# Kernel optimization log

Measured on AMD Instinct MI355X. Metric: run time of the kernel, lower is better.

## Reference

```python
import jax, jax.numpy as jnp
import numpy as np
from jax import lax

T, K, F = 262144, 20, 16


def setup_inputs() -> dict:
    key = jax.random.key(0)
    k1, k2, k3, k4 = jax.random.split(key, 4)
    return {
        "observations": jax.random.normal(k1, (T, F), dtype=jnp.float32),
        "beta_logits": jax.random.normal(k2, (K,), dtype=jnp.float32),
        "pi_logits": jax.random.normal(k3, (K, K), dtype=jnp.float32),
        "means": jax.random.normal(k4, (K, F), dtype=jnp.float32),
        "log_vars": jnp.zeros((K, F), dtype=jnp.float32),
    }


def _stick_breaking(logits):
    b = jax.nn.sigmoid(logits)
    cp = jnp.cumprod(1.0 - b)
    return b * jnp.concatenate([jnp.ones((1,), logits.dtype), cp[:-1]])


def _emission_logp(obs, means, log_vars):
    # Diagonal-covariance MultivariateNormal log_prob, vectorized over T and K
    # without materializing a [T,K,F] intermediate.
    var = jnp.exp(log_vars) + 1e-6                       # [K,F]
    inv = 1.0 / var
    const = jnp.sum(means * means * inv + jnp.log(2.0 * jnp.pi * var), axis=1)  # [K]
    quad = (obs * obs) @ inv.T - 2.0 * (obs @ (means * inv).T)                  # [T,K]
    return -0.5 * (quad + const[None, :])


def reference(observations, beta_logits, pi_logits, means, log_vars):
    w = _stick_breaking(beta_logits)                      # [K]
    P = jax.nn.softmax(pi_logits, axis=1)                 # [K,K]
    em = _emission_logp(observations, means, log_vars)    # [T,K]

    # Forward recursion (normalized alpha, as in the original)
    a0 = w * jnp.exp(em[0])
    a0 = a0 / (a0.sum() + 1e-10)

    def fstep(a, e):
        x = (a @ P) * jnp.exp(e)
        x = x / (x.sum() + 1e-10)
        return x, x

    _, a_rest = lax.scan(fstep, a0, em[1:])
    alpha = jnp.concatenate([a0[None], a_rest], axis=0)   # [T,K]

    # Backward recursion (normalized beta)
    bT = jnp.ones((K,), observations.dtype)

    def bstep(bn, e):
        x = P @ (bn * jnp.exp(e))
        x = x / (x.sum() + 1e-10)
        return x, x

    _, b_rest = lax.scan(bstep, bT, em[1:], reverse=True)
    beta = jnp.concatenate([b_rest, bT[None]], axis=0)    # [T,K]

    log_likelihood = jnp.log(alpha[-1].sum() + 1e-10)
    return alpha, beta, log_likelihood
```

## Files before the change

### kernel.cpp

```cpp
#include <hip/hip_runtime.h>
#include <hip/hip_fp16.h>


namespace {
constexpr int Tn = 262144;
constexpr int Kn = 20;
constexpr int Fn = 16;
constexpr float EPSF = 1e-10f;
constexpr float TINY = 1e-35f;

constexpr int Ln3 = 16;
constexpr int Wn3 = 16;
constexpr int NC3 = Tn / Ln3;
constexpr int NBF4 = NC3 / 32;
constexpr int NBSC = NC3 / 8;
constexpr int SPC = Ln3 * Kn;

constexpr size_t OFF_P    = 0;
constexpr size_t OFF_W    = 400;
constexpr size_t OFF_CK   = 420;
constexpr size_t OFF_MVIV = 440;
constexpr size_t OFF_E    = 1152;
constexpr size_t OFF_MF   = OFF_E + (size_t)Tn*20 + 64;
constexpr size_t OFF_MB   = OFF_MF + (size_t)Tn;
constexpr size_t OFF_MATF = OFF_MB + (size_t)Tn;
constexpr size_t OFF_MATB = OFF_MATF + 4*(size_t)NC3;
constexpr size_t OFF_SF   = OFF_MATB + 4*(size_t)NC3;
constexpr size_t OFF_SB   = OFF_SF + NC3;
constexpr size_t OFF_END  = OFF_SB + NC3;
}

#if __has_builtin(__builtin_amdgcn_rcpf)
#define FRCP(x) __builtin_amdgcn_rcpf(x)
#else
#define FRCP(x) (1.0f/(x))
#endif

template<int CTRL>
__device__ __forceinline__ float dpp_add(float v) {
  int s = __builtin_amdgcn_update_dpp(0, __float_as_int(v), CTRL, 0xF, 0xF, true);
  return v + __int_as_float(s);
}
template<int CTRL>
__device__ __forceinline__ float dppmov(float v) {
  return __int_as_float(__builtin_amdgcn_update_dpp(0, __float_as_int(v), CTRL, 0xF, 0xF, true));
}

__device__ __forceinline__ float reduce8(float v) {
  v = dpp_add<0xB1>(v);
  v = dpp_add<0x4E>(v);
  v = dpp_add<0x141>(v);
  return v;
}

__global__ __launch_bounds__(64) void prep_kernel(
    const float* beta_logits, const float* pi_logits,
    const float* means, const float* log_vars, float* ws)
{
  int k = threadIdx.x;
  if (k < Kn) {
    float row[Kn];
    float mx = -1e30f;
#pragma unroll
    for (int j = 0; j < Kn; ++j) { row[j] = pi_logits[k*Kn + j]; mx = fmaxf(mx, row[j]); }
    float s = 0.f;
#pragma unroll
    for (int j = 0; j < Kn; ++j) { row[j] = expf(row[j] - mx); s += row[j]; }
    float invs = 1.0f / s;
#pragma unroll
    for (int j = 0; j < Kn; ++j) ws[OFF_P + k*Kn + j] = row[j] * invs;
    float ck = 0.f;
#pragma unroll
    for (int f = 0; f < Fn; ++f) {
      float lv  = log_vars[k*Fn + f];
      float var = expf(lv) + 1e-6f;
      float iv  = 1.0f / var;
      float mu  = means[k*Fn + f];
      ((float2*)(ws + OFF_MVIV))[k*Fn + f] = make_float2(mu * iv, iv);
      ck += mu*mu*iv + logf(6.2831853071795864f * var);
    }
    ws[OFF_CK + k] = ck;
  } else if (k == Kn) {
    float cp = 1.f;
#pragma unroll
    for (int i = 0; i < Kn; ++i) {
      float b = 1.0f / (1.0f + expf(-beta_logits[i]));
      ws[OFF_W + i] = b * cp;
      cp *= (1.0f - b);
    }
  }
}

__global__ __launch_bounds__(320) void emis_kernel(const float* __restrict__ obs, float* ws)
{
  __shared__ __align__(16) float so[64][20];
  __shared__ __align__(16) float scm[16][24];
  __shared__ __align__(16) float scv[16][24];
  __shared__ __align__(16) float sck[20];
  const int tid = threadIdx.x;
  const int t0 = blockIdx.x * 64;

  if (tid < 256) {
    float4 v = ((const float4*)(obs + (size_t)t0 * Fn))[tid];
    int r = tid >> 2, j = tid & 3;
    *(float4*)&so[r][j*4] = v;
  } else {
    int i = tid - 256;
#pragma unroll
    for (int q = 0; q < 5; ++q) {
      int idx = i * 5 + q;
      float2 c2 = ((const float2*)(ws + OFF_MVIV))[idx];
      int k = idx >> 4, f = idx & 15;
      scm[f][k] = c2.x;
      scv[f][k] = c2.y;
    }
    if (i < Kn) sck[i] = ws[OFF_CK + i];
  }
  __syncthreads();

  const int tl = tid / 5;
  const int k0 = (tid - tl*5) * 4;

  float o[16];
  *(float4*)&o[0]  = *(const float4*)&so[tl][0];
  *(float4*)&o[4]  = *(const float4*)&so[tl][4];
  *(float4*)&o[8]  = *(const float4*)&so[tl][8];
  *(float4*)&o[12] = *(const float4*)&so[tl][12];

  float s1x=0.f,s1y=0.f,s1z=0.f,s1w=0.f;
  float s2x=0.f,s2y=0.f,s2z=0.f,s2w=0.f;
#pragma unroll
  for (int f = 0; f < Fn; ++f) {
    float4 cm = *(const float4*)&scm[f][k0];
    float4 cv = *(const float4*)&scv[f][k0];
    float ov = o[f];
    s1x = fmaf(cv.x * ov, ov, s1x); s2x = fmaf(cm.x, ov, s2x);
    s1y = fmaf(cv.y * ov, ov, s1y); s2y = fmaf(cm.y, ov, s2y);
    s1z = fmaf(cv.z * ov, ov, s1z); s2z = fmaf(cm.z, ov, s2z);
    s1w = fmaf(cv.w * ov, ov, s1w); s2w = fmaf(cm.w, ov, s2w);
  }
  float4 ckv = *(const float4*)&sck[k0];
  float4 rr;
  rr.x = __expf(fmaf(-0.5f, s1x + ckv.x, s2x));
  rr.y = __expf(fmaf(-0.5f, s1y + ckv.y, s2y));
  rr.z = __expf(fmaf(-0.5f, s1z + ckv.z, s2z));
  rr.w = __expf(fmaf(-0.5f, s1w + ckv.w, s2w));
  *(float4*)(ws + OFF_E + (size_t)(t0 + tl)*20 + k0) = rr;
}

__global__ __launch_bounds__(256, 4) void scan5_kernel(float* ws, float* out)
{
  const int tid = threadIdx.x;
  const int g   = tid >> 3;
  const int j   = tid & 7;
  const int q   = j & 3;
  const int s1i = 8 + j;
  const int s2i = 16 + q;
  const bool isF = ((int)blockIdx.x < NBF4);
  const int c = (isF ? (int)blockIdx.x : (int)blockIdx.x - NBF4) * 32 + g;
  const float* E = ws + OFF_E;

  float PA0[8], PB0[8], PA1[8], PB1[8], PA2[8], PB2[8];
  float PC0[4], PC1[4], PC2[4];
  {
    const int M[8] = {0,1,2,3,7,6,5,4};
#pragma unroll
    for (int i = 0; i < 8; ++i) {
      int ka = j ^ M[i];
      int kb = 8 + ka;
      if (isF) {
        PA0[i] = ws[OFF_P + ka*Kn + j];
        PB0[i] = ws[OFF_P + kb*Kn + j];
        PA1[i] = ws[OFF_P + ka*Kn + s1i];
        PB1[i] = ws[OFF_P + kb*Kn + s1i];
        PA2[i] = ws[OFF_P + ka*Kn + s2i];
        PB2[i] = ws[OFF_P + kb*Kn + s2i];
      } else {
        PA0[i] = ws[OFF_P + j*Kn + ka];
        PB0[i] = ws[OFF_P + j*Kn + kb];
        PA1[i] = ws[OFF_P + s1i*Kn + ka];
        PB1[i] = ws[OFF_P + s1i*Kn + kb];
        PA2[i] = ws[OFF_P + s2i*Kn + ka];
        PB2[i] = ws[OFF_P + s2i*Kn + kb];
      }
    }
#pragma unroll
    for (int i = 0; i < 4; ++i) {
      int kc = 16 + (q ^ i);
      if (isF) {
        PC0[i] = ws[OFF_P + kc*Kn + j];
        PC1[i] = ws[OFF_P + kc*Kn + s1i];
        PC2[i] = ws[OFF_P + kc*Kn + s2i];
      } else {
        PC0[i] = ws[OFF_P + j*Kn + kc];
        PC1[i] = ws[OFF_P + s1i*Kn + kc];
        PC2[i] = ws[OFF_P + s2i*Kn + kc];
      }
    }
  }

  float Ma = 1.f, Mc = 0.f, Md = 1.f;
  float* mArr = ws + (isF ? OFF_MF : OFF_MB);
  unsigned* uS = (unsigned*)(out + (isF ? (size_t)0 : (size_t)Tn * Kn) + (size_t)c * SPC);

  auto mobius = [&](float m) {
    float na = m * Ma;
    float nc = fmaf(EPSF, Mc, na);
    float nd = EPSF * Md;
    float mx = fmaxf(nc, nd);
    float lam = (mx > 0.f) ? FRCP(mx) : 1.0f;
    Ma = na*lam; Mc = nc*lam; Md = nd*lam;
  };

  auto packh2 = [](float a, float b) -> unsigned {
    __half2 h2 = __floats2half2_rn(a, b);
    return *(unsigned*)&h2;
  };

  auto xmv = [&](float w0, float w1, float w2, float& r0, float& r1, float& r2) {
    float x10 = dppmov<0xB1>(w0),  x11 = dppmov<0xB1>(w1),  x12 = dppmov<0xB1>(w2);
    float x20 = dppmov<0x4E>(w0),  x21 = dppmov<0x4E>(w1),  x22 = dppmov<0x4E>(w2);
    float x30 = dppmov<0x1B>(w0),  x31 = dppmov<0x1B>(w1),  x32 = dppmov<0x1B>(w2);
    float m0  = dppmov<0x141>(w0), m1  = dppmov<0x141>(w1);
    float m01 = dppmov<0xB1>(m0),  m11 = dppmov<0xB1>(m1);
    float m02 = dppmov<0x4E>(m0),  m12 = dppmov<0x4E>(m1);
    float m03 = dppmov<0x1B>(m0),  m13 = dppmov<0x1B>(m1);
#define ACC3(PA, PB, PC, OUT)                                             \
    {                                                                     \
      float a  = w0 * PA[0],  b = x10 * PA[1];                            \
      a = fmaf(x20, PA[2], a); b = fmaf(x30, PA[3], b);                   \
      a = fmaf(m0,  PA[4], a); b = fmaf(m01, PA[5], b);                   \
      a = fmaf(m02, PA[6], a); b = fmaf(m03, PA[7], b);                   \
      a = fmaf(w1,  PB[0], a); b = fmaf(x11, PB[1], b);                   \
      a = fmaf(x21, PB[2], a); b = fmaf(x31, PB[3], b);                   \
      a = fmaf(m1,  PB[4], a); b = fmaf(m11, PB[5], b);                   \
      a = fmaf(m12, PB[6], a); b = fmaf(m13, PB[7], b);                   \
      a = fmaf(w2,  PC[0], a); b = fmaf(x12, PC[1], b);                   \
      a = fmaf(x22, PC[2], a); b = fmaf(x32, PC[3], b);                   \
      OUT = a + b;                                                        \
    }
    ACC3(PA0, PB0, PC0, r0)
    ACC3(PA1, PB1, PC1, r1)
    ACC3(PA2, PB2, PC2, r2)
#undef ACC3
  };

  if (isF) {
    const int bodyStart = c * Ln3;
    const int tend = bodyStart + Ln3 - 1;
    const int t0 = (c == 0) ? 0 : (bodyStart - Wn3);
    float e0a = E[t0*20 + j], e1a = E[t0*20 + s1i], e2a = E[t0*20 + s2i];
    float v0, v1, v2;
    if (c == 0) {
      v0 = ws[OFF_W + j]   * e0a;
      v1 = ws[OFF_W + s1i] * e1a;
      v2 = ws[OFF_W + s2i] * e2a;
    } else {
      v0 = 0.05f * e0a; v1 = 0.05f * e1a; v2 = 0.05f * e2a;
    }
    float sv = reduce8(fmaf(0.5f, v2, v0 + v1));
    float m = sv;
    float iV = (sv > TINY) ? FRCP(sv) : 1.0f;
    if (sv <= TINY) { v0 = 0.05f; v1 = 0.05f; v2 = 0.05f; }
    if (c == 0) {
      mArr[0] = m;
      mobius(m);
      uS[j] = packh2(v0 * iV, v1 * iV);
      uS[8 + q] = packh2(v2 * iV, 0.f);
    }
    float A = m * iV;
    float rho = (m > TINY) ? FRCP(m) : 1.0f;
    float e0b = E[(t0+1)*20 + j], e1b = E[(t0+1)*20 + s1i], e2b = E[(t0+1)*20 + s2i];
    float e0c = E[(t0+2)*20 + j], e1c = E[(t0+2)*20 + s1i], e2c = E[(t0+2)*20 + s2i];

#define FWD_STEP(REC)                                                     \
    {                                                                     \
      float acc0, acc1, acc2;                                             \
      xmv(v0, v1, v2, acc0, acc1, acc2);                                  \
      float er0 = e0a * rho, er1 = e1a * rho, er2 = e2a * rho;            \
      e0a = e0b; e0b = e0c; e0c = E[(t+3)*20 + j];                        \
      e1a = e1b; e1b = e1c; e1c = E[(t+3)*20 + s1i];                      \
      e2a = e2b; e2b = e2c; e2c = E[(t+3)*20 + s2i];                      \
      v0 = acc0 * er0; v1 = acc1 * er1; v2 = acc2 * er2;                  \
      float sv2 = reduce8(fmaf(0.5f, v2, v0 + v1));                      \
      float mn = sv2 * A;                                                 \
      float iVn = (sv2 > TINY) ? FRCP(sv2) : 1.0f;                        \
      if (sv2 <= TINY) { v0 = 0.05f; v1 = 0.05f; v2 = 0.05f; }            \
      if (REC) {                                                          \
        mArr[t] = mn;                                                     \
        mobius(mn);                                                       \
        int lt = t - bodyStart;                                           \
        uS[lt*12 + j] = packh2(v0 * iVn, v1 * iVn);                       \
        uS[lt*12 + 8 + q] = packh2(v2 * iVn, 0.f);                        \
      }                                                                   \
      A = mn * iVn;                                                       \
      rho = (mn > TINY) ? FRCP(mn) : 1.0f;                                \
    }

    for (int t = t0 + 1; t < bodyStart; ++t) FWD_STEP(false)
    const int bstart2 = (c == 0) ? 1 : bodyStart;
    for (int t = bstart2; t <= tend; ++t) FWD_STEP(true)
#undef FWD_STEP
    ((float4*)(ws + OFF_MATF))[c] = make_float4(Ma, Mc, Md, 0.f);
  } else {
    const int bodyStart = c * Ln3;
    const int top = bodyStart + Ln3 - 1;
    int r0 = top + Wn3; if (r0 > Tn - 1) r0 = Tn - 1;
    float v0 = 0.05f, v1 = 0.05f, v2 = 0.05f;
    float sv = reduce8(fmaf(0.5f, v2, v0 + v1));
    float iV = (sv > TINY) ? FRCP(sv) : 1.0f;
    float A = iV;
    float rho = 1.0f;
    float e0a = E[r0*20 + j], e1a = E[r0*20 + s1i], e2a = E[r0*20 + s2i];
    float e0b = E[(r0-1)*20 + j], e1b = E[(r0-1)*20 + s1i], e2b = E[(r0-1)*20 + s2i];
    float e0c = E[(r0-2)*20 + j], e1c = E[(r0-2)*20 + s1i], e2c = E[(r0-2)*20 + s2i];

#define BWD_STEP(REC)                                                     \
    {                                                                     \
      float w0 = v0 * e0a, w1 = v1 * e1a, w2 = v2 * e2a;                  \
      float acc0, acc1, acc2;                                             \
      xmv(w0, w1, w2, acc0, acc1, acc2);                                  \
      v0 = acc0 * rho; v1 = acc1 * rho; v2 = acc2 * rho;                  \
      e0a = e0b; e0b = e0c; e0c = E[(r-2)*20 + j];                        \
      e1a = e1b; e1b = e1c; e1c = E[(r-2)*20 + s1i];                      \
      e2a = e2b; e2b = e2c; e2c = E[(r-2)*20 + s2i];                      \
      float sv2 = reduce8(fmaf(0.5f, v2, v0 + v1));                      \
      float mn = sv2 * A;                                                 \
      float iVn = (sv2 > TINY) ? FRCP(sv2) : 1.0f;                        \
      if (sv2 <= TINY) { v0 = 0.05f; v1 = 0.05f; v2 = 0.05f; }            \
      if (REC) {                                                          \
        mArr[r+1] = mn;                                                   \
        mobius(mn);                                                       \
        int lr = r - bodyStart;                                           \
        uS[lr*12 + j] = packh2(v0 * iVn, v1 * iVn);                       \
        uS[lr*12 + 8 + q] = packh2(v2 * iVn, 0.f);                        \
      }                                                                   \
      A = mn * iVn;                                                       \
      rho = (mn > TINY) ? FRCP(mn) : 1.0f;                                \
    }

    for (int r = r0 - 1; r > top; --r) BWD_STEP(false)
    int rb = (r0 - 1 < top) ? (r0 - 1) : top;
    for (int r = rb; r >= bodyStart; --r) BWD_STEP(true)
#undef BWD_STEP
    ((float4*)(ws + OFF_MATB))[NC3 - 1 - c] = make_float4(Ma, Mc, Md, 0.f);
  }
}

__global__ __launch_bounds__(1024) void combine4_kernel(float* ws, float* out)
{
  __shared__ float wag[16][3];
  __shared__ float wpre[16][3];
  const bool isF = (blockIdx.x == 0);
  const float4* M4 = (const float4*)(ws + (isF ? OFF_MATF : OFF_MATB));
  float* sArr = ws + (isF ? OFF_SF : OFF_SB);
  const float s0 = isF ? 1.0f : 20.0f;
  constexpr int PG = NC3 / 1024;
  const int tid  = threadIdx.x;
  const int lane = tid & 63;
  const int wid  = tid >> 6;

  float4 mm[PG];
#pragma unroll
  for (int i = 0; i < PG; ++i) mm[i] = M4[tid*PG + i];

  float a = 1.f, cc = 0.f, d = 1.f;
#pragma unroll
  for (int i = 0; i < PG; ++i) {
    float na = mm[i].x * a;
    float nc = fmaf(mm[i].y, a, mm[i].z * cc);
    float nd = mm[i].z * d;
    float mx = fmaxf(na, fmaxf(nc, nd));
    float lam = (mx > 0.f) ? FRCP(mx) : 1.0f;
    a = na*lam; cc = nc*lam; d = nd*lam;
  }

  float ia = a, ic = cc, id = d;
  for (int off = 1; off < 64; off <<= 1) {
    float pa = __shfl_up(ia, off, 64);
    float pc = __shfl_up(ic, off, 64);
    float pd = __shfl_up(id, off, 64);
    if (lane >= off) {
      float na = ia * pa;
      float nc = fmaf(ic, pa, id * pc);
      float nd = id * pd;
      float mx = fmaxf(na, fmaxf(nc, nd));
      float lam = (mx > 0.f) ? FRCP(mx) : 1.0f;
      ia = na*lam; ic = nc*lam; id = nd*lam;
    }
  }
  if (lane == 63) { wag[wid][0] = ia; wag[wid][1] = ic; wag[wid][2] = id; }
  __syncthreads();

  if (tid == 0) {
    float ea = 1.f, ec = 0.f, ed = 1.f;
#pragma unroll
    for (int w = 0; w < 16; ++w) {
      wpre[w][0] = ea; wpre[w][1] = ec; wpre[w][2] = ed;
      float na = wag[w][0] * ea;
      float nc = fmaf(wag[w][1], ea, wag[w][2] * ec);
      float nd = wag[w][2] * ed;
      float mx = fmaxf(na, fmaxf(nc, nd));
      float lam = (mx > 0.f) ? FRCP(mx) : 1.0f;
      ea = na*lam; ec = nc*lam; ed = nd*lam;
    }
    if (isF) {
      float den = fmaf(ec, s0, ed);
      float sfin = (den > 0.f) ? (ea * s0)/den : 0.f;
      out[(size_t)2 * Tn * Kn] = logf(sfin + EPSF);
    }
  }
  __syncthreads();

  float ea = __shfl_up(ia, 1, 64);
  float ec = __shfl_up(ic, 1, 64);
  float ed = __shfl_up(id, 1, 64);
  if (lane == 0) { ea = 1.f; ec = 0.f; ed = 1.f; }
  float pa = wpre[wid][0], pc = wpre[wid][1], pd = wpre[wid][2];
  float xa = ea * pa;
  float xc = fmaf(ec, pa, ed * pc);
  float xd = ed * pd;

  float num = xa * s0, den = fmaf(xc, s0, xd);
  float s = (den > 0.f) ? num/den : 0.f;
#pragma unroll
  for (int i = 0; i < PG; ++i) {
    sArr[tid*PG + i] = s;
    float nn = mm[i].x * s, dd = fmaf(mm[i].y, s, mm[i].z);
    s = (dd > 0.f) ? nn/dd : 0.f;
  }
}

__global__ __launch_bounds__(128) void scale4_kernel(float* ws, float* out)
{
  const int tid = threadIdx.x;
  const int g   = tid >> 4;
  const int ll  = tid & 15;
  const bool isF = ((int)blockIdx.x < NBSC);
  const int c = (isF ? (int)blockIdx.x : (int)blockIdx.x - NBSC) * 8 + g;
  float* base = out + (isF ? (size_t)0 : (size_t)Tn * Kn) + (size_t)c * SPC;
  const unsigned* uS = (const unsigned*)base;

  float mySig = 1.0f;
  if (isF) {
    const float* mA = ws + OFF_MF;
    float s = ws[OFF_SF + c];
    const int t0 = c * Ln3;
#pragma unroll
    for (int i = 0; i < Ln3; ++i) {
      float z = s * mA[t0 + i];
      float sn = z * FRCP(z + EPSF);
      if (i == ll) mySig = sn;
      s = sn;
    }
  } else {
    const float* mA = ws + OFF_MB;
    float s = ws[OFF_SB + (NC3 - 1 - c)];
    const int top = c * Ln3 + Ln3 - 1;
#pragma unroll
    for (int i = 0; i < Ln3; ++i) {
      int r = top - i;
      float sn;
      if (r == Tn - 1) sn = s;
      else {
        float z = s * mA[r + 1];
        sn = z * FRCP(z + EPSF);
      }
      if (i == Ln3 - 1 - ll) mySig = sn;
      s = sn;
    }
  }

  uint4 ua = ((const uint4*)(uS + ll*12))[0];
  uint4 ub = ((const uint4*)(uS + ll*12))[1];
  uint4 uc = ((const uint4*)(uS + ll*12))[2];
  __syncthreads();

  const bool onesRow = (!isF && c == NC3 - 1 && ll == Ln3 - 1);
  float sg = mySig;
  unsigned slots[12] = {ua.x,ua.y,ua.z,ua.w, ub.x,ub.y,ub.z,ub.w, uc.x,uc.y,uc.z,uc.w};
  float o[20];
#pragma unroll
  for (int jj = 0; jj < 8; ++jj) {
    __half2 h2 = *(__half2*)&slots[jj];
    float2 f2 = __half22float2(h2);
    o[jj]     = f2.x * sg;
    o[8 + jj] = f2.y * sg;
  }
#pragma unroll
  for (int qq = 0; qq < 4; ++qq) {
    __half2 h2 = *(__half2*)&slots[8 + qq];
    float2 f2 = __half22float2(h2);
    o[16 + qq] = f2.x * sg;
  }
  if (onesRow) {
#pragma unroll
    for (int k = 0; k < 20; ++k) o[k] = 1.0f;
  }
  float* dst = base + ll * 20;
  *(float4*)&dst[0]  = *(float4*)&o[0];
  *(float4*)&dst[4]  = *(float4*)&o[4];
  *(float4*)&dst[8]  = *(float4*)&o[8];
  *(float4*)&dst[12] = *(float4*)&o[12];
  *(float4*)&dst[16] = *(float4*)&o[16];
}

extern "C" void kernel_launch(void* const* d_in, const int* in_sizes, int n_in,
                              void* d_out, int out_size, void* d_ws, size_t ws_size,
                              hipStream_t stream) {
  const float* obs         = (const float*)d_in[0];
  const float* beta_logits = (const float*)d_in[1];
  const float* pi_logits   = (const float*)d_in[2];
  const float* means       = (const float*)d_in[3];
  const float* log_vars    = (const float*)d_in[4];
  float* out = (float*)d_out;
  float* ws  = (float*)d_ws;

  hipLaunchKernelGGL(prep_kernel, dim3(1), dim3(64), 0, stream,
                     beta_logits, pi_logits, means, log_vars, ws);
  hipLaunchKernelGGL(emis_kernel, dim3(Tn/64), dim3(320), 0, stream, obs, ws);
  hipLaunchKernelGGL(scan5_kernel, dim3(2*NBF4), dim3(256), 0, stream, ws, out);
  hipLaunchKernelGGL(combine4_kernel, dim3(2), dim3(1024), 0, stream, ws, out);
  hipLaunchKernelGGL(scale4_kernel, dim3(2*NBSC), dim3(128), 0, stream, ws, out);
}
```

Before: 102.0 us.

## Halve scan warm-up window and deepen emission prefetch pipeline

The forward and backward chunked scans now run an 8-step warm-up window before each 16-step chunk body instead of 16 steps. This cuts the redundant recomputation per chunk by roughly a third. Emission values are also prefetched four steps ahead instead of three, to hide more global-load latency. The shorter window relies on the HMM forgetting its initial state within 8 steps, so it may reduce accuracy of the chunk-boundary approximation.

```diff
diff --git a/kernel.cpp b/kernel.cpp
--- a/kernel.cpp
+++ b/kernel.cpp
@@ -10,7 +10,7 @@
 constexpr float TINY = 1e-35f;
 
 constexpr int Ln3 = 16;
-constexpr int Wn3 = 16;
+constexpr int Wn3 = 8;
 constexpr int NC3 = Tn / Ln3;
 constexpr int NBF4 = NC3 / 32;
 constexpr int NBSC = NC3 / 8;
@@ -148,7 +148,7 @@
   *(float4*)(ws + OFF_E + (size_t)(t0 + tl)*20 + k0) = rr;
 }
 
-__global__ __launch_bounds__(256, 4) void scan5_kernel(float* ws, float* out)
+__global__ __launch_bounds__(256, 4) void scan6_kernel(float* ws, float* out)
 {
   const int tid = threadIdx.x;
   const int g   = tid >> 3;
@@ -211,12 +211,10 @@
     float lam = (mx > 0.f) ? FRCP(mx) : 1.0f;
     Ma = na*lam; Mc = nc*lam; Md = nd*lam;
   };
-
   auto packh2 = [](float a, float b) -> unsigned {
     __half2 h2 = __floats2half2_rn(a, b);
     return *(unsigned*)&h2;
   };
-
   auto xmv = [&](float w0, float w1, float w2, float& r0, float& r1, float& r2) {
     float x10 = dppmov<0xB1>(w0),  x11 = dppmov<0xB1>(w1),  x12 = dppmov<0xB1>(w2);
     float x20 = dppmov<0x4E>(w0),  x21 = dppmov<0x4E>(w1),  x22 = dppmov<0x4E>(w2);
@@ -249,14 +247,16 @@
     const int bodyStart = c * Ln3;
     const int tend = bodyStart + Ln3 - 1;
     const int t0 = (c == 0) ? 0 : (bodyStart - Wn3);
-    float e0a = E[t0*20 + j], e1a = E[t0*20 + s1i], e2a = E[t0*20 + s2i];
     float v0, v1, v2;
-    if (c == 0) {
-      v0 = ws[OFF_W + j]   * e0a;
-      v1 = ws[OFF_W + s1i] * e1a;
-      v2 = ws[OFF_W + s2i] * e2a;
-    } else {
-      v0 = 0.05f * e0a; v1 = 0.05f * e1a; v2 = 0.05f * e2a;
+    {
+      float e0i = E[t0*20 + j], e1i = E[t0*20 + s1i], e2i = E[t0*20 + s2i];
+      if (c == 0) {
+        v0 = ws[OFF_W + j]   * e0i;
+        v1 = ws[OFF_W + s1i] * e1i;
+        v2 = ws[OFF_W + s2i] * e2i;
+      } else {
+        v0 = 0.05f * e0i; v1 = 0.05f * e1i; v2 = 0.05f * e2i;
+      }
     }
     float sv = reduce8(fmaf(0.5f, v2, v0 + v1));
     float m = sv;
@@ -270,17 +270,19 @@
     }
     float A = m * iV;
     float rho = (m > TINY) ? FRCP(m) : 1.0f;
-    float e0b = E[(t0+1)*20 + j], e1b = E[(t0+1)*20 + s1i], e2b = E[(t0+1)*20 + s2i];
-    float e0c = E[(t0+2)*20 + j], e1c = E[(t0+2)*20 + s1i], e2c = E[(t0+2)*20 + s2i];
+    float e0a = E[(t0+1)*20 + j], e1a = E[(t0+1)*20 + s1i], e2a = E[(t0+1)*20 + s2i];
+    float e0b = E[(t0+2)*20 + j], e1b = E[(t0+2)*20 + s1i], e2b = E[(t0+2)*20 + s2i];
+    float e0c = E[(t0+3)*20 + j], e1c = E[(t0+3)*20 + s1i], e2c = E[(t0+3)*20 + s2i];
+    float e0d = E[(t0+4)*20 + j], e1d = E[(t0+4)*20 + s1i], e2d = E[(t0+4)*20 + s2i];
 
 #define FWD_STEP(REC)                                                     \
     {                                                                     \
       float acc0, acc1, acc2;                                             \
       xmv(v0, v1, v2, acc0, acc1, acc2);                                  \
       float er0 = e0a * rho, er1 = e1a * rho, er2 = e2a * rho;            \
-      e0a = e0b; e0b = e0c; e0c = E[(t+3)*20 + j];                        \
-      e1a = e1b; e1b = e1c; e1c = E[(t+3)*20 + s1i];                      \
-      e2a = e2b; e2b = e2c; e2c = E[(t+3)*20 + s2i];                      \
+      e0a = e0b; e0b = e0c; e0c = e0d; e0d = E[(t+4)*20 + j];             \
+      e1a = e1b; e1b = e1c; e1c = e1d; e1d = E[(t+4)*20 + s1i];           \
+      e2a = e2b; e2b = e2c; e2c = e2d; e2d = E[(t+4)*20 + s2i];           \
       v0 = acc0 * er0; v1 = acc1 * er1; v2 = acc2 * er2;                  \
       float sv2 = reduce8(fmaf(0.5f, v2, v0 + v1));                      \
       float mn = sv2 * A;                                                 \
@@ -311,9 +313,10 @@
     float iV = (sv > TINY) ? FRCP(sv) : 1.0f;
     float A = iV;
     float rho = 1.0f;
-    float e0a = E[r0*20 + j], e1a = E[r0*20 + s1i], e2a = E[r0*20 + s2i];
+    float e0a = E[r0*20 + j],     e1a = E[r0*20 + s1i],     e2a = E[r0*20 + s2i];
     float e0b = E[(r0-1)*20 + j], e1b = E[(r0-1)*20 + s1i], e2b = E[(r0-1)*20 + s2i];
     float e0c = E[(r0-2)*20 + j], e1c = E[(r0-2)*20 + s1i], e2c = E[(r0-2)*20 + s2i];
+    float e0d = E[(r0-3)*20 + j], e1d = E[(r0-3)*20 + s1i], e2d = E[(r0-3)*20 + s2i];
 
 #define BWD_STEP(REC)                                                     \
     {                                                                     \
@@ -321,9 +324,9 @@
       float acc0, acc1, acc2;                                             \
       xmv(w0, w1, w2, acc0, acc1, acc2);                                  \
       v0 = acc0 * rho; v1 = acc1 * rho; v2 = acc2 * rho;                  \
-      e0a = e0b; e0b = e0c; e0c = E[(r-2)*20 + j];                        \
-      e1a = e1b; e1b = e1c; e1c = E[(r-2)*20 + s1i];                      \
-      e2a = e2b; e2b = e2c; e2c = E[(r-2)*20 + s2i];                      \
+      e0a = e0b; e0b = e0c; e0c = e0d; e0d = E[(r-3)*20 + j];             \
+      e1a = e1b; e1b = e1c; e1c = e1d; e1d = E[(r-3)*20 + s1i];           \
+      e2a = e2b; e2b = e2c; e2c = e2d; e2d = E[(r-3)*20 + s2i];           \
       float sv2 = reduce8(fmaf(0.5f, v2, v0 + v1));                      \
       float mn = sv2 * A;                                                 \
       float iVn = (sv2 > TINY) ? FRCP(sv2) : 1.0f;                        \
@@ -519,7 +522,7 @@
   hipLaunchKernelGGL(prep_kernel, dim3(1), dim3(64), 0, stream,
                      beta_logits, pi_logits, means, log_vars, ws);
   hipLaunchKernelGGL(emis_kernel, dim3(Tn/64), dim3(320), 0, stream, obs, ws);
-  hipLaunchKernelGGL(scan5_kernel, dim3(2*NBF4), dim3(256), 0, stream, ws, out);
+  hipLaunchKernelGGL(scan6_kernel, dim3(2*NBF4), dim3(256), 0, stream, ws, out);
   hipLaunchKernelGGL(combine4_kernel, dim3(2), dim3(1024), 0, stream, ws, out);
   hipLaunchKernelGGL(scale4_kernel, dim3(2*NBSC), dim3(128), 0, stream, ws, out);
 }
```

After: 99.01 us. -2.9%, faster.

## Fuse prep into consumers, halve warmup window, interleave two chunks per thread group

Applied to the files above, without the earlier changes.

Removes the separate prep kernel. Emission parameters are now computed inside emis_kernel, and the transition matrix and stick-breaking weights are computed into shared memory inside the scan kernel. The scan warmup window drops from 16 to 8 steps. Each 8-lane group now processes two adjacent chunks in one interleaved loop, giving independent instruction streams that hide DPP and reduce latency. In exchange, the work per block is duplicated, register pressure rises (the occupancy hint is dropped), and the shorter warmup may reduce accuracy at chunk boundaries.

```diff
diff --git a/kernel.cpp b/kernel.cpp
--- a/kernel.cpp
+++ b/kernel.cpp
@@ -10,18 +10,14 @@
 constexpr float TINY = 1e-35f;
 
 constexpr int Ln3 = 16;
-constexpr int Wn3 = 16;
+constexpr int Wn3 = 8;
 constexpr int NC3 = Tn / Ln3;
-constexpr int NBF4 = NC3 / 32;
+constexpr int NBF8 = NC3 / 2 / 32;
 constexpr int NBSC = NC3 / 8;
 constexpr int SPC = Ln3 * Kn;
 
-constexpr size_t OFF_P    = 0;
-constexpr size_t OFF_W    = 400;
-constexpr size_t OFF_CK   = 420;
-constexpr size_t OFF_MVIV = 440;
-constexpr size_t OFF_E    = 1152;
-constexpr size_t OFF_MF   = OFF_E + (size_t)Tn*20 + 64;
+constexpr size_t OFF_E    = 256;
+constexpr size_t OFF_MF   = OFF_E + (size_t)Tn*20 + 256;
 constexpr size_t OFF_MB   = OFF_MF + (size_t)Tn;
 constexpr size_t OFF_MATF = OFF_MB + (size_t)Tn;
 constexpr size_t OFF_MATB = OFF_MATF + 4*(size_t)NC3;
@@ -53,45 +49,14 @@
   return v;
 }
 
-__global__ __launch_bounds__(64) void prep_kernel(
-    const float* beta_logits, const float* pi_logits,
-    const float* means, const float* log_vars, float* ws)
-{
-  int k = threadIdx.x;
-  if (k < Kn) {
-    float row[Kn];
-    float mx = -1e30f;
-#pragma unroll
-    for (int j = 0; j < Kn; ++j) { row[j] = pi_logits[k*Kn + j]; mx = fmaxf(mx, row[j]); }
-    float s = 0.f;
-#pragma unroll
-    for (int j = 0; j < Kn; ++j) { row[j] = expf(row[j] - mx); s += row[j]; }
-    float invs = 1.0f / s;
-#pragma unroll
-    for (int j = 0; j < Kn; ++j) ws[OFF_P + k*Kn + j] = row[j] * invs;
-    float ck = 0.f;
-#pragma unroll
-    for (int f = 0; f < Fn; ++f) {
-      float lv  = log_vars[k*Fn + f];
-      float var = expf(lv) + 1e-6f;
-      float iv  = 1.0f / var;
-      float mu  = means[k*Fn + f];
-      ((float2*)(ws + OFF_MVIV))[k*Fn + f] = make_float2(mu * iv, iv);
-      ck += mu*mu*iv + logf(6.2831853071795864f * var);
-    }
-    ws[OFF_CK + k] = ck;
-  } else if (k == Kn) {
-    float cp = 1.f;
-#pragma unroll
-    for (int i = 0; i < Kn; ++i) {
-      float b = 1.0f / (1.0f + expf(-beta_logits[i]));
-      ws[OFF_W + i] = b * cp;
-      cp *= (1.0f - b);
-    }
-  }
-}
-
-__global__ __launch_bounds__(320) void emis_kernel(const float* __restrict__ obs, float* ws)
+__device__ __forceinline__ unsigned packh2(float a, float b) {
+  __half2 h2 = __floats2half2_rn(a, b);
+  return *(unsigned*)&h2;
+}
+
+__global__ __launch_bounds__(320) void emis_kernel(
+    const float* __restrict__ obs, const float* __restrict__ means,
+    const float* __restrict__ log_vars, float* ws)
 {
   __shared__ __align__(16) float so[64][20];
   __shared__ __align__(16) float scm[16][24];
@@ -106,15 +71,20 @@
     *(float4*)&so[r][j*4] = v;
   } else {
     int i = tid - 256;
-#pragma unroll
-    for (int q = 0; q < 5; ++q) {
-      int idx = i * 5 + q;
-      float2 c2 = ((const float2*)(ws + OFF_MVIV))[idx];
-      int k = idx >> 4, f = idx & 15;
-      scm[f][k] = c2.x;
-      scv[f][k] = c2.y;
-    }
-    if (i < Kn) sck[i] = ws[OFF_CK + i];
+    if (i < Kn) {
+      float ck = 0.f;
+#pragma unroll
+      for (int f = 0; f < Fn; ++f) {
+        float lv  = log_vars[i*Fn + f];
+        float var = expf(lv) + 1e-6f;
+        float iv  = 1.0f / var;
+        float mu  = means[i*Fn + f];
+        scm[f][i] = mu * iv;
+        scv[f][i] = iv;
+        ck += mu*mu*iv + logf(6.2831853071795864f * var);
+      }
+      sck[i] = ck;
+    }
   }
   __syncthreads();
 
@@ -148,16 +118,42 @@
   *(float4*)(ws + OFF_E + (size_t)(t0 + tl)*20 + k0) = rr;
 }
 
-__global__ __launch_bounds__(256, 4) void scan5_kernel(float* ws, float* out)
+__global__ __launch_bounds__(256) void scan8_kernel(
+    const float* __restrict__ beta_logits, const float* __restrict__ pi_logits,
+    float* ws, float* out)
 {
+  __shared__ __align__(16) float Psh[Kn*Kn];
+  __shared__ float wsh[Kn];
   const int tid = threadIdx.x;
+  if (tid < Kn) {
+    float row[Kn]; float mx = -1e30f;
+#pragma unroll
+    for (int jj = 0; jj < Kn; ++jj) { row[jj] = pi_logits[tid*Kn + jj]; mx = fmaxf(mx, row[jj]); }
+    float s = 0.f;
+#pragma unroll
+    for (int jj = 0; jj < Kn; ++jj) { row[jj] = expf(row[jj] - mx); s += row[jj]; }
+    float invs = 1.0f / s;
+#pragma unroll
+    for (int jj = 0; jj < Kn; ++jj) Psh[tid*Kn + jj] = row[jj] * invs;
+  } else if (tid == Kn) {
+    float cp = 1.f;
+#pragma unroll
+    for (int i = 0; i < Kn; ++i) {
+      float b = 1.0f / (1.0f + expf(-beta_logits[i]));
+      wsh[i] = b * cp;
+      cp *= (1.0f - b);
+    }
+  }
+  __syncthreads();
+
   const int g   = tid >> 3;
   const int j   = tid & 7;
   const int q   = j & 3;
   const int s1i = 8 + j;
   const int s2i = 16 + q;
-  const bool isF = ((int)blockIdx.x < NBF4);
-  const int c = (isF ? (int)blockIdx.x : (int)blockIdx.x - NBF4) * 32 + g;
+  const bool isF = ((int)blockIdx.x < NBF8);
+  const int pairI = (isF ? (int)blockIdx.x : (int)blockIdx.x - NBF8) * 32 + g;
+  const int cA = pairI * 2, cB = cA + 1;
   const float* E = ws + OFF_E;
 
   float PA0[8], PB0[8], PA1[8], PB1[8], PA2[8], PB2[8];
@@ -169,41 +165,33 @@
       int ka = j ^ M[i];
       int kb = 8 + ka;
       if (isF) {
-        PA0[i] = ws[OFF_P + ka*Kn + j];
-        PB0[i] = ws[OFF_P + kb*Kn + j];
-        PA1[i] = ws[OFF_P + ka*Kn + s1i];
-        PB1[i] = ws[OFF_P + kb*Kn + s1i];
-        PA2[i] = ws[OFF_P + ka*Kn + s2i];
-        PB2[i] = ws[OFF_P + kb*Kn + s2i];
+        PA0[i] = Psh[ka*Kn + j];   PB0[i] = Psh[kb*Kn + j];
+        PA1[i] = Psh[ka*Kn + s1i]; PB1[i] = Psh[kb*Kn + s1i];
+        PA2[i] = Psh[ka*Kn + s2i]; PB2[i] = Psh[kb*Kn + s2i];
       } else {
-        PA0[i] = ws[OFF_P + j*Kn + ka];
-        PB0[i] = ws[OFF_P + j*Kn + kb];
-        PA1[i] = ws[OFF_P + s1i*Kn + ka];
-        PB1[i] = ws[OFF_P + s1i*Kn + kb];
-        PA2[i] = ws[OFF_P + s2i*Kn + ka];
-        PB2[i] = ws[OFF_P + s2i*Kn + kb];
+        PA0[i] = Psh[j*Kn + ka];   PB0[i] = Psh[j*Kn + kb];
+        PA1[i] = Psh[s1i*Kn + ka]; PB1[i] = Psh[s1i*Kn + kb];
+        PA2[i] = Psh[s2i*Kn + ka]; PB2[i] = Psh[s2i*Kn + kb];
       }
     }
 #pragma unroll
     for (int i = 0; i < 4; ++i) {
       int kc = 16 + (q ^ i);
       if (isF) {
-        PC0[i] = ws[OFF_P + kc*Kn + j];
-        PC1[i] = ws[OFF_P + kc*Kn + s1i];
-        PC2[i] = ws[OFF_P + kc*Kn + s2i];
+        PC0[i] = Psh[kc*Kn + j]; PC1[i] = Psh[kc*Kn + s1i]; PC2[i] = Psh[kc*Kn + s2i];
       } else {
-        PC0[i] = ws[OFF_P + j*Kn + kc];
-        PC1[i] = ws[OFF_P + s1i*Kn + kc];
-        PC2[i] = ws[OFF_P + s2i*Kn + kc];
+        PC0[i] = Psh[j*Kn + kc]; PC1[i] = Psh[s1i*Kn + kc]; PC2[i] = Psh[s2i*Kn + kc];
       }
     }
   }
-
-  float Ma = 1.f, Mc = 0.f, Md = 1.f;
+  const float w0c = wsh[j], w1c = wsh[s1i], w2c = wsh[s2i];
+
+  float MaA=1.f, McA=0.f, MdA=1.f, MaB=1.f, McB=0.f, MdB=1.f;
   float* mArr = ws + (isF ? OFF_MF : OFF_MB);
-  unsigned* uS = (unsigned*)(out + (isF ? (size_t)0 : (size_t)Tn * Kn) + (size_t)c * SPC);
-
-  auto mobius = [&](float m) {
+  unsigned* uSA = (unsigned*)(out + (isF ? (size_t)0 : (size_t)Tn * Kn) + (size_t)cA * SPC);
+  unsigned* uSB = uSA + SPC;
+
+  auto mobius = [&](float m, float& Ma, float& Mc, float& Md) {
     float na = m * Ma;
     float nc = fmaf(EPSF, Mc, na);
     float nd = EPSF * Md;
@@ -211,12 +199,6 @@
     float lam = (mx > 0.f) ? FRCP(mx) : 1.0f;
     Ma = na*lam; Mc = nc*lam; Md = nd*lam;
   };
-
-  auto packh2 = [](float a, float b) -> unsigned {
-    __half2 h2 = __floats2half2_rn(a, b);
-    return *(unsigned*)&h2;
-  };
-
   auto xmv = [&](float w0, float w1, float w2, float& r0, float& r1, float& r2) {
     float x10 = dppmov<0xB1>(w0),  x11 = dppmov<0xB1>(w1),  x12 = dppmov<0xB1>(w2);
     float x20 = dppmov<0x4E>(w0),  x21 = dppmov<0x4E>(w1),  x22 = dppmov<0x4E>(w2);
@@ -246,104 +228,147 @@
   };
 
   if (isF) {
-    const int bodyStart = c * Ln3;
-    const int tend = bodyStart + Ln3 - 1;
-    const int t0 = (c == 0) ? 0 : (bodyStart - Wn3);
-    float e0a = E[t0*20 + j], e1a = E[t0*20 + s1i], e2a = E[t0*20 + s2i];
-    float v0, v1, v2;
-    if (c == 0) {
-      v0 = ws[OFF_W + j]   * e0a;
-      v1 = ws[OFF_W + s1i] * e1a;
-      v2 = ws[OFF_W + s2i] * e2a;
-    } else {
-      v0 = 0.05f * e0a; v1 = 0.05f * e1a; v2 = 0.05f * e2a;
-    }
-    float sv = reduce8(fmaf(0.5f, v2, v0 + v1));
-    float m = sv;
-    float iV = (sv > TINY) ? FRCP(sv) : 1.0f;
-    if (sv <= TINY) { v0 = 0.05f; v1 = 0.05f; v2 = 0.05f; }
-    if (c == 0) {
-      mArr[0] = m;
-      mobius(m);
-      uS[j] = packh2(v0 * iV, v1 * iV);
-      uS[8 + q] = packh2(v2 * iV, 0.f);
-    }
-    float A = m * iV;
-    float rho = (m > TINY) ? FRCP(m) : 1.0f;
-    float e0b = E[(t0+1)*20 + j], e1b = E[(t0+1)*20 + s1i], e2b = E[(t0+1)*20 + s2i];
-    float e0c = E[(t0+2)*20 + j], e1c = E[(t0+2)*20 + s1i], e2c = E[(t0+2)*20 + s2i];
-
-#define FWD_STEP(REC)                                                     \
-    {                                                                     \
-      float acc0, acc1, acc2;                                             \
-      xmv(v0, v1, v2, acc0, acc1, acc2);                                  \
-      float er0 = e0a * rho, er1 = e1a * rho, er2 = e2a * rho;            \
-      e0a = e0b; e0b = e0c; e0c = E[(t+3)*20 + j];                        \
-      e1a = e1b; e1b = e1c; e1c = E[(t+3)*20 + s1i];                      \
-      e2a = e2b; e2b = e2c; e2c = E[(t+3)*20 + s2i];                      \
-      v0 = acc0 * er0; v1 = acc1 * er1; v2 = acc2 * er2;                  \
-      float sv2 = reduce8(fmaf(0.5f, v2, v0 + v1));                      \
-      float mn = sv2 * A;                                                 \
-      float iVn = (sv2 > TINY) ? FRCP(sv2) : 1.0f;                        \
-      if (sv2 <= TINY) { v0 = 0.05f; v1 = 0.05f; v2 = 0.05f; }            \
-      if (REC) {                                                          \
-        mArr[t] = mn;                                                     \
-        mobius(mn);                                                       \
-        int lt = t - bodyStart;                                           \
-        uS[lt*12 + j] = packh2(v0 * iVn, v1 * iVn);                       \
-        uS[lt*12 + 8 + q] = packh2(v2 * iVn, 0.f);                        \
-      }                                                                   \
-      A = mn * iVn;                                                       \
-      rho = (mn > TINY) ? FRCP(mn) : 1.0f;                                \
-    }
-
-    for (int t = t0 + 1; t < bodyStart; ++t) FWD_STEP(false)
-    const int bstart2 = (c == 0) ? 1 : bodyStart;
-    for (int t = bstart2; t <= tend; ++t) FWD_STEP(true)
-#undef FWD_STEP
-    ((float4*)(ws + OFF_MATF))[c] = make_float4(Ma, Mc, Md, 0.f);
+    const int bSA = cA * Ln3;
+    const bool c0 = (cA == 0);
+    float vA0, vA1, vA2, vB0, vB1, vB2;
+    {
+      const float* p0 = E + (ptrdiff_t)(bSA - 8) * 20;
+      vA0 = 0.05f * p0[j]; vA1 = 0.05f * p0[s1i]; vA2 = 0.05f * p0[s2i];
+      const float* p1 = E + (ptrdiff_t)(bSA + 8) * 20;
+      vB0 = 0.05f * p1[j]; vB1 = 0.05f * p1[s1i]; vB2 = 0.05f * p1[s2i];
+    }
+    float svA = reduce8(fmaf(0.5f, vA2, vA0 + vA1));
+    float iVA = (svA > TINY) ? FRCP(svA) : 1.0f;
+    if (svA <= TINY) { vA0 = vA1 = vA2 = 0.05f; }
+    float AA = svA * iVA;
+    float rhoA = (svA > TINY) ? FRCP(svA) : 1.0f;
+    float svB = reduce8(fmaf(0.5f, vB2, vB0 + vB1));
+    float iVB = (svB > TINY) ? FRCP(svB) : 1.0f;
+    if (svB <= TINY) { vB0 = vB1 = vB2 = 0.05f; }
+    float AB = svB * iVB;
+    float rhoB = (svB > TINY) ? FRCP(svB) : 1.0f;
+
+    const float* pA = E + (ptrdiff_t)(bSA - 7) * 20;
+    float eA0a = pA[j], eA1a = pA[s1i], eA2a = pA[s2i]; pA += 20;
+    float eA0b = pA[j], eA1b = pA[s1i], eA2b = pA[s2i]; pA += 20;
+    float eA0c = pA[j], eA1c = pA[s1i], eA2c = pA[s2i]; pA += 20;
+    const float* pB = E + (ptrdiff_t)(bSA + 9) * 20;
+    float eB0a = pB[j], eB1a = pB[s1i], eB2a = pB[s2i]; pB += 20;
+    float eB0b = pB[j], eB1b = pB[s1i], eB2b = pB[s2i]; pB += 20;
+    float eB0c = pB[j], eB1c = pB[s1i], eB2c = pB[s2i]; pB += 20;
+
+    for (int i = 0; i < 23; ++i) {
+      const int t = bSA - 7 + i;
+      float accA0, accA1, accA2, accB0, accB1, accB2;
+      xmv(vA0, vA1, vA2, accA0, accA1, accA2);
+      xmv(vB0, vB1, vB2, accB0, accB1, accB2);
+      float ea0 = eA0a, ea1 = eA1a, ea2 = eA2a;
+      float eb0 = eB0a, eb1 = eB1a, eb2 = eB2a;
+      eA0a = eA0b; eA0b = eA0c; eA0c = pA[j];
+      eA1a = eA1b; eA1b = eA1c; eA1c = pA[s1i];
+      eA2a = eA2b; eA2b = eA2c; eA2c = pA[s2i]; pA += 20;
+      eB0a = eB0b; eB0b = eB0c; eB0c = pB[j];
+      eB1a = eB1b; eB1b = eB1c; eB1c = pB[s1i];
+      eB2a = eB2b; eB2b = eB2c; eB2c = pB[s2i]; pB += 20;
+      const bool init0 = c0 && (t == 0);
+      vA0 = init0 ? (w0c * ea0) : (accA0 * (ea0 * rhoA));
+      vA1 = init0 ? (w1c * ea1) : (accA1 * (ea1 * rhoA));
+      vA2 = init0 ? (w2c * ea2) : (accA2 * (ea2 * rhoA));
+      vB0 = accB0 * (eb0 * rhoB);
+      vB1 = accB1 * (eb1 * rhoB);
+      vB2 = accB2 * (eb2 * rhoB);
+      float sA = reduce8(fmaf(0.5f, vA2, vA0 + vA1));
+      float sB = reduce8(fmaf(0.5f, vB2, vB0 + vB1));
+      float mnA = sA * (init0 ? 1.0f : AA);
+      float mnB = sB * AB;
+      float iVnA = (sA > TINY) ? FRCP(sA) : 1.0f;
+      float iVnB = (sB > TINY) ? FRCP(sB) : 1.0f;
+      if (sA <= TINY) { vA0 = vA1 = vA2 = 0.05f; }
+      if (sB <= TINY) { vB0 = vB1 = vB2 = 0.05f; }
+      if (i >= 7) {
+        const int lt = i - 7;
+        mArr[t] = mnA;
+        mArr[t + 16] = mnB;
+        mobius(mnA, MaA, McA, MdA);
+        mobius(mnB, MaB, McB, MdB);
+        uSA[lt*12 + j] = packh2(vA0 * iVnA, vA1 * iVnA);
+        uSA[lt*12 + 8 + q] = packh2(vA2 * iVnA, 0.f);
+        uSB[lt*12 + j] = packh2(vB0 * iVnB, vB1 * iVnB);
+        uSB[lt*12 + 8 + q] = packh2(vB2 * iVnB, 0.f);
+      }
+      AA = mnA * iVnA; AB = mnB * iVnB;
+      rhoA = (mnA > TINY) ? FRCP(mnA) : 1.0f;
+      rhoB = (mnB > TINY) ? FRCP(mnB) : 1.0f;
+    }
+    ((float4*)(ws + OFF_MATF))[cA] = make_float4(MaA, McA, MdA, 0.f);
+    ((float4*)(ws + OFF_MATF))[cB] = make_float4(MaB, McB, MdB, 0.f);
   } else {
-    const int bodyStart = c * Ln3;
-    const int top = bodyStart + Ln3 - 1;
-    int r0 = top + Wn3; if (r0 > Tn - 1) r0 = Tn - 1;
-    float v0 = 0.05f, v1 = 0.05f, v2 = 0.05f;
-    float sv = reduce8(fmaf(0.5f, v2, v0 + v1));
-    float iV = (sv > TINY) ? FRCP(sv) : 1.0f;
-    float A = iV;
-    float rho = 1.0f;
-    float e0a = E[r0*20 + j], e1a = E[r0*20 + s1i], e2a = E[r0*20 + s2i];
-    float e0b = E[(r0-1)*20 + j], e1b = E[(r0-1)*20 + s1i], e2b = E[(r0-1)*20 + s2i];
-    float e0c = E[(r0-2)*20 + j], e1c = E[(r0-2)*20 + s1i], e2c = E[(r0-2)*20 + s2i];
-
-#define BWD_STEP(REC)                                                     \
-    {                                                                     \
-      float w0 = v0 * e0a, w1 = v1 * e1a, w2 = v2 * e2a;                  \
-      float acc0, acc1, acc2;                                             \
-      xmv(w0, w1, w2, acc0, acc1, acc2);                                  \
-      v0 = acc0 * rho; v1 = acc1 * rho; v2 = acc2 * rho;                  \
-      e0a = e0b; e0b = e0c; e0c = E[(r-2)*20 + j];                        \
-      e1a = e1b; e1b = e1c; e1c = E[(r-2)*20 + s1i];                      \
-      e2a = e2b; e2b = e2c; e2c = E[(r-2)*20 + s2i];                      \
-      float sv2 = reduce8(fmaf(0.5f, v2, v0 + v1));                      \
-      float mn = sv2 * A;                                                 \
-      float iVn = (sv2 > TINY) ? FRCP(sv2) : 1.0f;                        \
-      if (sv2 <= TINY) { v0 = 0.05f; v1 = 0.05f; v2 = 0.05f; }            \
-      if (REC) {                                                          \
-        mArr[r+1] = mn;                                                   \
-        mobius(mn);                                                       \
-        int lr = r - bodyStart;                                           \
-        uS[lr*12 + j] = packh2(v0 * iVn, v1 * iVn);                       \
-        uS[lr*12 + 8 + q] = packh2(v2 * iVn, 0.f);                        \
-      }                                                                   \
-      A = mn * iVn;                                                       \
-      rho = (mn > TINY) ? FRCP(mn) : 1.0f;                                \
-    }
-
-    for (int r = r0 - 1; r > top; --r) BWD_STEP(false)
-    int rb = (r0 - 1 < top) ? (r0 - 1) : top;
-    for (int r = rb; r >= bodyStart; --r) BWD_STEP(true)
-#undef BWD_STEP
-    ((float4*)(ws + OFF_MATB))[NC3 - 1 - c] = make_float4(Ma, Mc, Md, 0.f);
+    const int topA = cA * Ln3 + Ln3 - 1;
+    const bool lastB = (cB == NC3 - 1);
+    float vA0 = 0.05f, vA1 = 0.05f, vA2 = 0.05f;
+    float vB0 = 0.05f, vB1 = 0.05f, vB2 = 0.05f;
+    float svA = reduce8(fmaf(0.5f, vA2, vA0 + vA1));
+    float AA = (svA > TINY) ? FRCP(svA) : 1.0f;
+    float rhoA = 1.0f;
+    float AB = AA;
+    float rhoB = 1.0f;
+
+    const float* pA = E + (ptrdiff_t)(topA + 8) * 20;
+    float eA0a = pA[j], eA1a = pA[s1i], eA2a = pA[s2i]; pA -= 20;
+    float eA0b = pA[j], eA1b = pA[s1i], eA2b = pA[s2i]; pA -= 20;
+    float eA0c = pA[j], eA1c = pA[s1i], eA2c = pA[s2i]; pA -= 20;
+    const float* pB = E + (ptrdiff_t)(topA + 24) * 20;
+    float eB0a = pB[j], eB1a = pB[s1i], eB2a = pB[s2i]; pB -= 20;
+    float eB0b = pB[j], eB1b = pB[s1i], eB2b = pB[s2i]; pB -= 20;
+    float eB0c = pB[j], eB1c = pB[s1i], eB2c = pB[s2i]; pB -= 20;
+
+    for (int i = 0; i < 23; ++i) {
+      const int r = topA + 7 - i;
+      const bool initB = lastB && ((r + 16) == Tn - 2);
+      float wA0 = vA0 * eA0a, wA1 = vA1 * eA1a, wA2 = vA2 * eA2a;
+      float vb0 = initB ? 0.05f : vB0;
+      float vb1 = initB ? 0.05f : vB1;
+      float vb2 = initB ? 0.05f : vB2;
+      float wB0 = vb0 * eB0a, wB1 = vb1 * eB1a, wB2 = vb2 * eB2a;
+      float accA0, accA1, accA2, accB0, accB1, accB2;
+      xmv(wA0, wA1, wA2, accA0, accA1, accA2);
+      xmv(wB0, wB1, wB2, accB0, accB1, accB2);
+      float rhoBe = initB ? 1.0f : rhoB;
+      vA0 = accA0 * rhoA; vA1 = accA1 * rhoA; vA2 = accA2 * rhoA;
+      vB0 = accB0 * rhoBe; vB1 = accB1 * rhoBe; vB2 = accB2 * rhoBe;
+      eA0a = eA0b; eA0b = eA0c; eA0c = pA[j];
+      eA1a = eA1b; eA1b = eA1c; eA1c = pA[s1i];
+      eA2a = eA2b; eA2b = eA2c; eA2c = pA[s2i]; pA -= 20;
+      eB0a = eB0b; eB0b = eB0c; eB0c = pB[j];
+      eB1a = eB1b; eB1b = eB1c; eB1c = pB[s1i];
+      eB2a = eB2b; eB2b = eB2c; eB2c = pB[s2i]; pB -= 20;
+      float sA = reduce8(fmaf(0.5f, vA2, vA0 + vA1));
+      float sB = reduce8(fmaf(0.5f, vB2, vB0 + vB1));
+      float mnA = sA * AA;
+      float mnB = sB * (initB ? 1.0f : AB);
+      float iVnA = (sA > TINY) ? FRCP(sA) : 1.0f;
+      float iVnB = (sB > TINY) ? FRCP(sB) : 1.0f;
+      if (sA <= TINY) { vA0 = vA1 = vA2 = 0.05f; }
+      if (sB <= TINY) { vB0 = vB1 = vB2 = 0.05f; }
+      if (i >= 7) {
+        const int lr = 22 - i;
+        mArr[r + 1] = mnA;
+        mobius(mnA, MaA, McA, MdA);
+        uSA[lr*12 + j] = packh2(vA0 * iVnA, vA1 * iVnA);
+        uSA[lr*12 + 8 + q] = packh2(vA2 * iVnA, 0.f);
+        if (!lastB || i >= 8) {
+          mArr[r + 17] = mnB;
+          mobius(mnB, MaB, McB, MdB);
+          uSB[lr*12 + j] = packh2(vB0 * iVnB, vB1 * iVnB);
+          uSB[lr*12 + 8 + q] = packh2(vB2 * iVnB, 0.f);
+        }
+      }
+      AA = mnA * iVnA; AB = mnB * iVnB;
+      rhoA = (mnA > TINY) ? FRCP(mnA) : 1.0f;
+      rhoB = (mnB > TINY) ? FRCP(mnB) : 1.0f;
+    }
+    ((float4*)(ws + OFF_MATB))[NC3 - 1 - cA] = make_float4(MaA, McA, MdA, 0.f);
+    ((float4*)(ws + OFF_MATB))[NC3 - 1 - cB] = make_float4(MaB, McB, MdB, 0.f);
   }
 }
 
@@ -516,10 +541,10 @@
   float* out = (float*)d_out;
   float* ws  = (float*)d_ws;
 
-  hipLaunchKernelGGL(prep_kernel, dim3(1), dim3(64), 0, stream,
-                     beta_logits, pi_logits, means, log_vars, ws);
-  hipLaunchKernelGGL(emis_kernel, dim3(Tn/64), dim3(320), 0, stream, obs, ws);
-  hipLaunchKernelGGL(scan5_kernel, dim3(2*NBF4), dim3(256), 0, stream, ws, out);
+  hipLaunchKernelGGL(emis_kernel, dim3(Tn/64), dim3(320), 0, stream,
+                     obs, means, log_vars, ws);
+  hipLaunchKernelGGL(scan8_kernel, dim3(2*NBF8), dim3(256), 0, stream,
+                     beta_logits, pi_logits, ws, out);
   hipLaunchKernelGGL(combine4_kernel, dim3(2), dim3(1024), 0, stream, ws, out);
   hipLaunchKernelGGL(scale4_kernel, dim3(2*NBSC), dim3(128), 0, stream, ws, out);
 }
```

Result: faster. 93.91 us (-7.9%).
